# Performance work log

Measured on AMD Instinct MI355X. Metric: run time of the kernel, lower is better.

Reference implementation:

```python
import jax, jax.numpy as jnp
import numpy as np

N = 100000
NEG_SLOPE = 0.2

def _leaky_relu(x, slope):
    return jnp.where(x >= 0, x, slope * x)

def _gat_layer(h_in, W, a_src, a_dst, b, src, dst, heads, out_ch):
    # h: [N, H, C]
    h = (h_in @ W).reshape(-1, heads, out_ch)
    alpha_src = (h * a_src).sum(-1)  # [N, H]
    alpha_dst = (h * a_dst).sum(-1)  # [N, H]
    e = _leaky_relu(alpha_src[src] + alpha_dst[dst], NEG_SLOPE)  # [E, H]
    # segment softmax over destination nodes
    m = jax.ops.segment_max(e, dst, num_segments=N)
    m = jnp.where(jnp.isfinite(m), m, 0.0)
    ex = jnp.exp(e - m[dst])
    denom = jax.ops.segment_sum(ex, dst, num_segments=N)
    attn = ex / (denom[dst] + 1e-16)  # [E, H]
    out = jax.ops.segment_sum(h[src] * attn[:, :, None], dst, num_segments=N)  # [N, H, C]
    return out.reshape(-1, heads * out_ch) + b

def setup_inputs() -> dict:
    key = jax.random.key(0)
    ks = jax.random.split(key, 10)
    F_in, H1, C1, n_cls = 512, 8, 8, 16
    E = 1600000
    x = jax.random.normal(ks[0], (N, F_in), dtype=jnp.float32)
    edge_index = jax.random.randint(ks[1], (2, E), 0, N, dtype=jnp.int64)
    s1 = 1.0 / np.sqrt(F_in)
    W1 = jax.random.uniform(ks[2], (F_in, H1 * C1), jnp.float32, -s1, s1)
    a1_src = jax.random.normal(ks[3], (H1, C1), dtype=jnp.float32) * 0.1
    a1_dst = jax.random.normal(ks[4], (H1, C1), dtype=jnp.float32) * 0.1
    b1 = jnp.zeros((H1 * C1,), jnp.float32)
    s2 = 1.0 / np.sqrt(H1 * C1)
    W2 = jax.random.uniform(ks[5], (H1 * C1, n_cls), jnp.float32, -s2, s2)
    a2_src = jax.random.normal(ks[6], (1, n_cls), dtype=jnp.float32) * 0.1
    a2_dst = jax.random.normal(ks[7], (1, n_cls), dtype=jnp.float32) * 0.1
    b2 = jnp.zeros((n_cls,), jnp.float32)
    return {"x": x, "edge_index": edge_index, "W1": W1, "a1_src": a1_src,
            "a1_dst": a1_dst, "b1": b1, "W2": W2, "a2_src": a2_src,
            "a2_dst": a2_dst, "b2": b2}

def reference(x, edge_index, W1, a1_src, a1_dst, b1, W2, a2_src, a2_dst, b2):
    # add self loops (GATConv default)
    loops = jnp.arange(N, dtype=edge_index.dtype)
    src = jnp.concatenate([edge_index[0], loops])
    dst = jnp.concatenate([edge_index[1], loops])
    h = _gat_layer(x, W1, a1_src, a1_dst, b1, src, dst, 8, 8)
    h = jax.nn.elu(h)
    out = _gat_layer(h, W2, a2_src, a2_dst, b2, src, dst, 1, 16)
    return jax.nn.log_softmax(out, axis=1)
```

## Files before the change

### kernel.cpp

```cpp
#include <hip/hip_runtime.h>
#include <math.h>

#define NEG_SLOPE 0.2f
#define BKT_SHIFT 8
#define BKT_RANGE 256
#define EPB 4096

typedef __attribute__((ext_vector_type(8))) short bf16x8;
typedef __attribute__((ext_vector_type(4))) float f32x4;

__device__ __forceinline__ float elu1(float x)  { return x > 0.f ? x : expm1f(x); }

__device__ __forceinline__ unsigned short f2bf(float f) {
  unsigned u = __float_as_uint(f);
  unsigned r = (u + 0x7FFFu + ((u >> 16) & 1u)) >> 16;
  return (unsigned short)r;
}
__device__ __forceinline__ float bflo(unsigned u) { return __uint_as_float(u << 16); }
__device__ __forceinline__ float bfhi(unsigned u) { return __uint_as_float(u & 0xFFFF0000u); }
__device__ __forceinline__ unsigned cvt_pk_bf16(float lo, float hi) {
  unsigned r;
  asm("v_cvt_pk_bf16_f32 %0, %1, %2" : "=v"(r) : "v"(lo), "v"(hi));
  return r;
}

__global__ __launch_bounds__(256) void k_cvtW_zero(const float* __restrict__ W,
                                                   unsigned short* __restrict__ Wt,
                                                   int* __restrict__ bucketCount) {
  int i = blockIdx.x * 256 + threadIdx.x;
  if (i < 1024) bucketCount[i] = 0;
  if (i >= 512 * 64) return;
  int k = i >> 6, c = i & 63;
  Wt[(size_t)c * 512 + k] = f2bf(W[i]);
}

__global__ __launch_bounds__(256) void k_gemm1_mfma(const float* __restrict__ x,
                                                    const unsigned short* __restrict__ Wt,
                                                    const float* __restrict__ a1s,
                                                    const float* __restrict__ a1d,
                                                    unsigned* __restrict__ h1f8,
                                                    unsigned* __restrict__ ef1sp,
                                                    unsigned* __restrict__ ef1dp, int N) {
  __shared__ __align__(16) unsigned short As[128 * 64];
  __shared__ __align__(16) unsigned short Bs[64 * 64];
  const int t = threadIdx.x;
  const int w = t >> 6;
  const int l = t & 63;
  const int fr = l & 15;
  const int fq = l >> 4;
  const int rowbase = blockIdx.x * 128;
  f32x4 acc[2][4] = {};

  for (int k0 = 0; k0 < 512; k0 += 64) {
#pragma unroll
    for (int j = 0; j < 8; ++j) {
      int idx = j * 256 + t;
      int row = idx >> 4;
      int cg  = idx & 15;
      int grow = rowbase + row;
      float4 v = make_float4(0.f, 0.f, 0.f, 0.f);
      if (grow < N) v = *(const float4*)(x + (size_t)grow * 512 + k0 + cg * 4);
      uint2 pk;
      pk.x = cvt_pk_bf16(v.x, v.y);
      pk.y = cvt_pk_bf16(v.z, v.w);
      int ch = cg >> 1;
      int pch = ch ^ (row & 7);
      *((uint2*)(As + row * 64 + pch * 8 + (cg & 1) * 4)) = pk;
    }
#pragma unroll
    for (int rep = 0; rep < 2; ++rep) {
      int i = t + rep * 256;
      int c = i >> 3, ch = i & 7;
      uint4 v = *(const uint4*)(Wt + (size_t)c * 512 + k0 + ch * 8);
      *((uint4*)(Bs + c * 64 + (ch ^ (c & 7)) * 8)) = v;
    }
    __syncthreads();
#pragma unroll
    for (int ks = 0; ks < 2; ++ks) {
      bf16x8 a[2], b[4];
#pragma unroll
      for (int m = 0; m < 2; ++m) {
        int r = w * 32 + m * 16 + fr;
        int ch = (ks * 4 + fq) ^ (r & 7);
        a[m] = *((const bf16x8*)(As + r * 64 + ch * 8));
      }
#pragma unroll
      for (int n = 0; n < 4; ++n) {
        int c = n * 16 + fr;
        int ch = (ks * 4 + fq) ^ (c & 7);
        b[n] = *((const bf16x8*)(Bs + c * 64 + ch * 8));
      }
#pragma unroll
      for (int m = 0; m < 2; ++m)
#pragma unroll
        for (int n = 0; n < 4; ++n)
          acc[m][n] = __builtin_amdgcn_mfma_f32_16x16x32_bf16(a[m], b[n], acc[m][n], 0, 0, 0);
    }
    __syncthreads();
  }

  float* Asf = (float*)As;
#pragma unroll
  for (int m = 0; m < 2; ++m) {
    if (m) __syncthreads();
#pragma unroll
    for (int reg = 0; reg < 4; ++reg) {
      int lrow = w * 16 + fq * 4 + reg;
#pragma unroll
      for (int n = 0; n < 4; ++n)
        Asf[lrow * 64 + n * 16 + fr] = acc[m][n][reg];
    }
    __syncthreads();
#pragma unroll
    for (int p = 0; p < 4; ++p) {
      int flat = p * 256 + t;
      int lrow = flat >> 4, j = flat & 15;
      int g = rowbase + ((lrow >> 4) << 5) + m * 16 + (lrow & 15);
      float4 f = *(float4*)(Asf + lrow * 64 + j * 4);
      unsigned u = __builtin_amdgcn_cvt_pk_fp8_f32(f.x, f.y, 0u, 0);
      u = __builtin_amdgcn_cvt_pk_fp8_f32(f.z, f.w, u, 1);
      if (g < N) h1f8[(size_t)g * 16 + j] = u;
    }
#pragma unroll
    for (int p = 0; p < 2; ++p) {
      int flat = p * 256 + t;
      int lrow = flat >> 3, hh = flat & 7;
      int g = rowbase + ((lrow >> 4) << 5) + m * 16 + (lrow & 15);
      float4 f0 = *(float4*)(Asf + lrow * 64 + hh * 8);
      float4 f1 = *(float4*)(Asf + lrow * 64 + hh * 8 + 4);
      const float* sa = a1s + hh * 8;
      const float* da = a1d + hh * 8;
      float ss = f0.x*sa[0]+f0.y*sa[1]+f0.z*sa[2]+f0.w*sa[3]
               + f1.x*sa[4]+f1.y*sa[5]+f1.z*sa[6]+f1.w*sa[7];
      float dd = f0.x*da[0]+f0.y*da[1]+f0.z*da[2]+f0.w*da[3]
               + f1.x*da[4]+f1.y*da[5]+f1.z*da[6]+f1.w*da[7];
      if (g < N) {
        ef1sp[(size_t)g * 8 + hh] = cvt_pk_bf16(expf(ss), expf(NEG_SLOPE * ss));
        ef1dp[(size_t)g * 8 + hh] = cvt_pk_bf16(expf(dd), expf(NEG_SLOPE * dd));
      }
    }
  }
}

__global__ __launch_bounds__(256) void k_bhist(const int* __restrict__ dst,
                                               int* __restrict__ bucketCount,
                                               int E, int B) {
  __shared__ int h[512];
  int t = threadIdx.x;
  for (int i = t; i < B; i += 256) h[i] = 0;
  __syncthreads();
  int e0 = blockIdx.x * EPB;
#pragma unroll
  for (int i = 0; i < EPB / 256; ++i) {
    int e = e0 + i * 256 + t;
    if (e < E) atomicAdd(&h[dst[e] >> BKT_SHIFT], 1);
  }
  __syncthreads();
  for (int i = t; i < B; i += 256)
    if (h[i]) atomicAdd(bucketCount + i, h[i]);
}

__global__ __launch_bounds__(512) void k_bscan(const int* __restrict__ bucketCount,
                                               int* __restrict__ bucketOff,
                                               int* __restrict__ gCursor, int B, int E) {
  __shared__ int sm[512];
  int t = threadIdx.x;
  int v = (t < B) ? bucketCount[t] : 0;
  sm[t] = v;
  __syncthreads();
  int acc = v;
#pragma unroll
  for (int o = 1; o < 512; o <<= 1) {
    int u = (t >= o) ? sm[t - o] : 0;
    __syncthreads();
    acc += u;
    sm[t] = acc;
    __syncthreads();
  }
  if (t < B) {
    bucketOff[t] = acc - v;
    gCursor[t] = acc - v;
  }
  if (t == 0) bucketOff[B] = E;
}

__global__ __launch_bounds__(256) void k_bin(const int* __restrict__ src,
                                             const int* __restrict__ dst,
                                             int* __restrict__ gCursor,
                                             unsigned* __restrict__ binned,
                                             int E, int B) {
  __shared__ int hist[512];
  __shared__ int base[512];
  int t = threadIdx.x;
  for (int i = t; i < B; i += 256) hist[i] = 0;
  __syncthreads();
  int e0 = blockIdx.x * EPB;
#pragma unroll
  for (int i = 0; i < EPB / 256; ++i) {
    int e = e0 + i * 256 + t;
    if (e < E) atomicAdd(&hist[dst[e] >> BKT_SHIFT], 1);
  }
  __syncthreads();
  for (int i = t; i < B; i += 256) {
    int c = hist[i];
    base[i] = c ? atomicAdd(gCursor + i, c) : 0;
    hist[i] = 0;
  }
  __syncthreads();
#pragma unroll
  for (int i = 0; i < EPB / 256; ++i) {
    int e = e0 + i * 256 + t;
    if (e < E) {
      int d = dst[e];
      int b = d >> BKT_SHIFT;
      int r = atomicAdd(&hist[b], 1);
      binned[base[b] + r] = ((unsigned)(d & (BKT_RANGE - 1)) << 24) | (unsigned)src[e];
    }
  }
}

__global__ __launch_bounds__(256) void k_build(const int* __restrict__ bucketOff,
                                               const unsigned* __restrict__ binned,
                                               int* __restrict__ rowptr,
                                               int* __restrict__ deg,
                                               int* __restrict__ srt, int N) {
  __shared__ int ldeg[BKT_RANGE];
  __shared__ int sm[BKT_RANGE];
  __shared__ int lcur[BKT_RANGE];
  int t = threadIdx.x;
  int b = blockIdx.x;
  int nbase = b * BKT_RANGE;
  int estart = bucketOff[b];
  int eend = bucketOff[b + 1];
  ldeg[t] = 0;
  __syncthreads();
  for (int e = estart + t; e < eend; e += 256)
    atomicAdd(&ldeg[binned[e] >> 24], 1);
  __syncthreads();
  int v = ldeg[t];
  sm[t] = v;
  __syncthreads();
  int acc = v;
#pragma unroll
  for (int o = 1; o < 256; o <<= 1) {
    int u = (t >= o) ? sm[t - o] : 0;
    __syncthreads();
    acc += u;
    sm[t] = acc;
    __syncthreads();
  }
  int excl = estart + acc - v;
  int node = nbase + t;
  if (node < N) {
    rowptr[node] = excl;
    deg[node] = v;
  }
  lcur[t] = excl;
  __syncthreads();
  for (int e = estart + t; e < eend; e += 256) {
    unsigned p = binned[e];
    int pos = atomicAdd(&lcur[p >> 24], 1);
    srt[pos] = (int)(p & 0xFFFFFFu);
  }
}

__global__ __launch_bounds__(256) void k_agg1f(const int* __restrict__ rowptr,
                                               const int* __restrict__ deg,
                                               const int* __restrict__ srt,
                                               const unsigned* __restrict__ ef1sp,
                                               const unsigned* __restrict__ ef1dp,
                                               const unsigned* __restrict__ h1f8,
                                               const float* __restrict__ b1,
                                               const float* __restrict__ W2,
                                               const float* __restrict__ a2s,
                                               const float* __restrict__ a2d,
                                               unsigned short* __restrict__ h2b,
                                               unsigned* __restrict__ ef2sp,
                                               float* __restrict__ ef2d, int N) {
  __shared__ float vsm[4][64];
  const int t = threadIdx.x;
  const int w = t >> 6;
  const int lane = t & 63;
  const int wid = blockIdx.x * 4 + w;
  const int slot = lane >> 4;
  const int c4 = lane & 15;
  const int h = c4 >> 1;
  float a2sr = a2s[c4];
  float a2dr = a2d[c4];
  float wreg[16];
#pragma unroll
  for (int m = 0; m < 16; ++m) wreg[m] = W2[(slot * 16 + m) * 16 + c4];
  float4 b1v = *(const float4*)(b1 + c4 * 4);
  if (wid >= N) return;
  const int d = wid;

  unsigned ddu = ef1dp[(size_t)d * 8 + h];
  float ddx = bflo(ddu), ddy = bfhi(ddu);
  unsigned es0 = ef1sp[(size_t)d * 8 + h];
  unsigned sv = h1f8[(size_t)d * 16 + c4];
  float ex0 = fmaxf(bflo(es0) * ddx, bfhi(es0) * ddy);
  ex0 = (slot == 0) ? ex0 : 0.f;
  float a0 = ex0 * __builtin_amdgcn_cvt_f32_fp8(sv, 0);
  float a1 = ex0 * __builtin_amdgcn_cvt_f32_fp8(sv, 1);
  float a2 = ex0 * __builtin_amdgcn_cvt_f32_fp8(sv, 2);
  float a3 = ex0 * __builtin_amdgcn_cvt_f32_fp8(sv, 3);
  float den = ex0;

  int start = rowptr[d];
  int len = deg[d];
  for (int kb = 0; kb < len; kb += 64) {
    int li = kb + lane;
    int sreg = (li < len) ? srt[start + li] : 0;
    int nit = min(16, (len - kb + 3) >> 2);
#pragma unroll 2
    for (int it = 0; it < nit; ++it) {
      int idx = kb + it * 4 + slot;
      int s = __shfl(sreg, it * 4 + slot);
      bool valid = idx < len;
      unsigned es = ef1sp[(size_t)s * 8 + h];
      unsigned hv = h1f8[(size_t)s * 16 + c4];
      float ex = fmaxf(bflo(es) * ddx, bfhi(es) * ddy);
      ex = valid ? ex : 0.f;
      a0 = fmaf(ex, __builtin_amdgcn_cvt_f32_fp8(hv, 0), a0);
      a1 = fmaf(ex, __builtin_amdgcn_cvt_f32_fp8(hv, 1), a1);
      a2 = fmaf(ex, __builtin_amdgcn_cvt_f32_fp8(hv, 2), a2);
      a3 = fmaf(ex, __builtin_amdgcn_cvt_f32_fp8(hv, 3), a3);
      den += ex;
    }
  }
#pragma unroll
  for (int o = 16; o < 64; o <<= 1) {
    a0 += __shfl_xor(a0, o);
    a1 += __shfl_xor(a1, o);
    a2 += __shfl_xor(a2, o);
    a3 += __shfl_xor(a3, o);
    den += __shfl_xor(den, o);
  }
  float rden = 1.f / (den + 1e-16f);
  if (slot == 0) {
    float4 vv;
    vv.x = elu1(a0 * rden + b1v.x);
    vv.y = elu1(a1 * rden + b1v.y);
    vv.z = elu1(a2 * rden + b1v.z);
    vv.w = elu1(a3 * rden + b1v.w);
    *(float4*)&vsm[w][c4 * 4] = vv;
  }
  float partial = 0.f;
#pragma unroll
  for (int m = 0; m < 16; ++m) partial = fmaf(vsm[w][slot * 16 + m], wreg[m], partial);
  float qs = partial * a2sr;
  float qd = partial * a2dr;
#pragma unroll
  for (int o = 1; o < 64; o <<= 1) {
    qs += __shfl_xor(qs, o);
    qd += __shfl_xor(qd, o);
  }
  float p2 = partial + __shfl_down(partial, 32);
  float hcv = p2 + __shfl_down(p2, 16);
  if (lane < 16) h2b[(size_t)d * 16 + c4] = f2bf(hcv);
  if (lane == 0) {
    ef2sp[d] = cvt_pk_bf16(expf(qs), expf(NEG_SLOPE * qs));
    *(float2*)(ef2d + (size_t)d * 2) = make_float2(expf(qd), expf(NEG_SLOPE * qd));
  }
}

__global__ __launch_bounds__(256) void k_agg2(const int* __restrict__ rowptr,
                                              const int* __restrict__ deg,
                                              const int* __restrict__ srt,
                                              const unsigned* __restrict__ ef2sp,
                                              const float* __restrict__ ef2d,
                                              const unsigned short* __restrict__ h2b,
                                              const float* __restrict__ b2,
                                              float* __restrict__ out, int N) {
  const int t = threadIdx.x;
  const int lane = t & 63;
  const int wid = (blockIdx.x * 256 + t) >> 6;
  const int slot = lane >> 2;
  const int cg = lane & 3;
  float4 b2v = *(const float4*)(b2 + cg * 4);
  if (wid >= N) return;
  const int d = wid;
  float2 ddp = *(const float2*)(ef2d + (size_t)d * 2);
  unsigned ps0 = ef2sp[d];
  uint2 sv = *(const uint2*)(h2b + (size_t)d * 16 + cg * 4);
  float ex0 = fmaxf(bflo(ps0) * ddp.x, bfhi(ps0) * ddp.y);
  ex0 = (slot == 0) ? ex0 : 0.f;
  float a0 = ex0 * bflo(sv.x), a1 = ex0 * bfhi(sv.x);
  float a2 = ex0 * bflo(sv.y), a3 = ex0 * bfhi(sv.y);
  float den = ex0;

  int start = rowptr[d];
  int len = deg[d];
  for (int kb = 0; kb < len; kb += 64) {
    int li = kb + lane;
    int sreg = (li < len) ? srt[start + li] : 0;
    int nit = min(4, (len - kb + 15) >> 4);
#pragma unroll 2
    for (int it = 0; it < nit; ++it) {
      int idx = kb + it * 16 + slot;
      int s = __shfl(sreg, it * 16 + slot);
      bool valid = idx < len;
      unsigned ps = ef2sp[s];
      uint2 hv = *(const uint2*)(h2b + (size_t)s * 16 + cg * 4);
      float ex = fmaxf(bflo(ps) * ddp.x, bfhi(ps) * ddp.y);
      ex = valid ? ex : 0.f;
      a0 = fmaf(ex, bflo(hv.x), a0);
      a1 = fmaf(ex, bfhi(hv.x), a1);
      a2 = fmaf(ex, bflo(hv.y), a2);
      a3 = fmaf(ex, bfhi(hv.y), a3);
      den += ex;
    }
  }
#pragma unroll
  for (int o = 4; o < 64; o <<= 1) {
    a0 += __shfl_xor(a0, o);
    a1 += __shfl_xor(a1, o);
    a2 += __shfl_xor(a2, o);
    a3 += __shfl_xor(a3, o);
    den += __shfl_xor(den, o);
  }
  float rden = 1.f / (den + 1e-16f);
  float v0 = a0 * rden + b2v.x;
  float v1 = a1 * rden + b2v.y;
  float v2 = a2 * rden + b2v.z;
  float v3 = a3 * rden + b2v.w;
  float m = fmaxf(fmaxf(v0, v1), fmaxf(v2, v3));
  m = fmaxf(m, __shfl_xor(m, 1));
  m = fmaxf(m, __shfl_xor(m, 2));
  float s = expf(v0 - m) + expf(v1 - m) + expf(v2 - m) + expf(v3 - m);
  s += __shfl_xor(s, 1);
  s += __shfl_xor(s, 2);
  float lse = m + logf(s);
  if (lane < 4) {
    float4 o4 = make_float4(v0 - lse, v1 - lse, v2 - lse, v3 - lse);
    *(float4*)(out + (size_t)d * 16 + cg * 4) = o4;
  }
}

extern "C" void kernel_launch(void* const* d_in, const int* in_sizes, int n_in,
                              void* d_out, int out_size, void* d_ws, size_t ws_size,
                              hipStream_t stream) {
  const float* x    = (const float*)d_in[0];
  const int*   ei   = (const int*)d_in[1];
  const float* W1   = (const float*)d_in[2];
  const float* a1s  = (const float*)d_in[3];
  const float* a1d  = (const float*)d_in[4];
  const float* b1   = (const float*)d_in[5];
  const float* W2   = (const float*)d_in[6];
  const float* a2s  = (const float*)d_in[7];
  const float* a2d  = (const float*)d_in[8];
  const float* b2   = (const float*)d_in[9];
  float* out = (float*)d_out;

  const int N = in_sizes[0] / 512;
  const int E = in_sizes[1] / 2;
  const int* src = ei;
  const int* dst = ei + E;
  const int B = (N + BKT_RANGE - 1) >> BKT_SHIFT;
  const int EB = (E + EPB - 1) / EPB;

  float* w = (float*)d_ws;
  float* ef2d = w;  w += (size_t)N * 2;
  unsigned* ef1sp = (unsigned*)w;  w += (size_t)N * 8;
  unsigned* ef1dp = (unsigned*)w;  w += (size_t)N * 8;
  unsigned* ef2sp = (unsigned*)w;  w += (size_t)N;
  unsigned* h1f8  = (unsigned*)w;  w += (size_t)N * 16;
  unsigned short* h2b = (unsigned short*)w;  w += (size_t)N * 8;
  unsigned short* Wt  = (unsigned short*)w;  w += 512 * 64 / 2;
  int* iw = (int*)w;
  int* deg         = iw;  iw += N;
  int* rowptr      = iw;  iw += N;
  int* bucketCount = iw;  iw += 1024;
  int* bucketOff   = iw;  iw += 1024;
  int* gCursor     = iw;  iw += 1024;
  int* srt         = iw;  iw += E;
  unsigned* binned = (unsigned*)iw;  iw += E;

  k_cvtW_zero<<<(512 * 64 + 255) / 256, 256, 0, stream>>>(W1, Wt, bucketCount);

  k_bhist<<<EB, 256, 0, stream>>>(dst, bucketCount, E, B);
  k_bscan<<<1, 512, 0, stream>>>(bucketCount, bucketOff, gCursor, B, E);
  k_bin<<<EB, 256, 0, stream>>>(src, dst, gCursor, binned, E, B);
  k_build<<<B, 256, 0, stream>>>(bucketOff, binned, rowptr, deg, srt, N);

  k_gemm1_mfma<<<(N + 127) / 128, 256, 0, stream>>>(x, Wt, a1s, a1d, h1f8, ef1sp, ef1dp, N);
  k_agg1f<<<(N + 3) / 4, 256, 0, stream>>>(rowptr, deg, srt, ef1sp, ef1dp, h1f8,
                                           b1, W2, a2s, a2d, h2b, ef2sp, ef2d, N);

  k_agg2<<<(N + 3) / 4, 256, 0, stream>>>(rowptr, deg, srt, ef2sp, ef2d, h2b, b2, out, N);
}
```

Baseline: 222.6 us.

## Interleave source attention and features, load GEMM A directly, fold bucket scan

Four separate changes. The GEMM now loads x rows straight into MFMA A-fragment registers instead of staging them through shared memory, which shrinks the LDS footprint. The per-source attention exponentials and the fp8 features are packed into one 24-word record per node, so each gathered edge in aggregation touches a single 96-byte region instead of two separate arrays. The standalone bucket scan kernel is removed and every k_bin and k_build block recomputes the prefix sum in shared memory, trading redundant work for one fewer launch; aggregation loops also get a higher unroll factor.

Result: faster. 212.0 us (-4.8%).

```diff
diff --git a/kernel.cpp b/kernel.cpp
--- a/kernel.cpp
+++ b/kernel.cpp
@@ -38,11 +38,11 @@
                                                     const unsigned short* __restrict__ Wt,
                                                     const float* __restrict__ a1s,
                                                     const float* __restrict__ a1d,
-                                                    unsigned* __restrict__ h1f8,
-                                                    unsigned* __restrict__ ef1sp,
+                                                    unsigned* __restrict__ hx,
                                                     unsigned* __restrict__ ef1dp, int N) {
-  __shared__ __align__(16) unsigned short As[128 * 64];
-  __shared__ __align__(16) unsigned short Bs[64 * 64];
+  __shared__ __align__(16) float Sm[64 * 64];
+  unsigned short* Bs = (unsigned short*)Sm;
+  float* Asf = Sm;
   const int t = threadIdx.x;
   const int w = t >> 6;
   const int l = t & 63;
@@ -51,22 +51,13 @@
   const int rowbase = blockIdx.x * 128;
   f32x4 acc[2][4] = {};
 
+  const int r0g = rowbase + w * 32 + fr;
+  const int r1g = r0g + 16;
+  const bool v0 = r0g < N, v1 = r1g < N;
+  const float* xr0 = x + (size_t)r0g * 512 + fq * 8;
+  const float* xr1 = x + (size_t)r1g * 512 + fq * 8;
+
   for (int k0 = 0; k0 < 512; k0 += 64) {
-#pragma unroll
-    for (int j = 0; j < 8; ++j) {
-      int idx = j * 256 + t;
-      int row = idx >> 4;
-      int cg  = idx & 15;
-      int grow = rowbase + row;
-      float4 v = make_float4(0.f, 0.f, 0.f, 0.f);
-      if (grow < N) v = *(const float4*)(x + (size_t)grow * 512 + k0 + cg * 4);
-      uint2 pk;
-      pk.x = cvt_pk_bf16(v.x, v.y);
-      pk.y = cvt_pk_bf16(v.z, v.w);
-      int ch = cg >> 1;
-      int pch = ch ^ (row & 7);
-      *((uint2*)(As + row * 64 + pch * 8 + (cg & 1) * 4)) = pk;
-    }
 #pragma unroll
     for (int rep = 0; rep < 2; ++rep) {
       int i = t + rep * 256;
@@ -74,16 +65,30 @@
       uint4 v = *(const uint4*)(Wt + (size_t)c * 512 + k0 + ch * 8);
       *((uint4*)(Bs + c * 64 + (ch ^ (c & 7)) * 8)) = v;
     }
+    bf16x8 a[2][2];
+#pragma unroll
+    for (int m = 0; m < 2; ++m) {
+      const float* xr = m ? xr1 : xr0;
+      bool vv = m ? v1 : v0;
+#pragma unroll
+      for (int ks = 0; ks < 2; ++ks) {
+        float4 f0 = make_float4(0.f, 0.f, 0.f, 0.f), f1 = f0;
+        if (vv) {
+          f0 = *(const float4*)(xr + k0 + ks * 32);
+          f1 = *(const float4*)(xr + k0 + ks * 32 + 4);
+        }
+        union { unsigned u[4]; bf16x8 v8; } un;
+        un.u[0] = cvt_pk_bf16(f0.x, f0.y);
+        un.u[1] = cvt_pk_bf16(f0.z, f0.w);
+        un.u[2] = cvt_pk_bf16(f1.x, f1.y);
+        un.u[3] = cvt_pk_bf16(f1.z, f1.w);
+        a[m][ks] = un.v8;
+      }
+    }
     __syncthreads();
 #pragma unroll
     for (int ks = 0; ks < 2; ++ks) {
-      bf16x8 a[2], b[4];
-#pragma unroll
-      for (int m = 0; m < 2; ++m) {
-        int r = w * 32 + m * 16 + fr;
-        int ch = (ks * 4 + fq) ^ (r & 7);
-        a[m] = *((const bf16x8*)(As + r * 64 + ch * 8));
-      }
+      bf16x8 b[4];
 #pragma unroll
       for (int n = 0; n < 4; ++n) {
         int c = n * 16 + fr;
@@ -94,12 +99,11 @@
       for (int m = 0; m < 2; ++m)
 #pragma unroll
         for (int n = 0; n < 4; ++n)
-          acc[m][n] = __builtin_amdgcn_mfma_f32_16x16x32_bf16(a[m], b[n], acc[m][n], 0, 0, 0);
-    }
-    __syncthreads();
-  }
-
-  float* Asf = (float*)As;
+          acc[m][n] = __builtin_amdgcn_mfma_f32_16x16x32_bf16(a[m][ks], b[n], acc[m][n], 0, 0, 0);
+    }
+    __syncthreads();
+  }
+
 #pragma unroll
   for (int m = 0; m < 2; ++m) {
     if (m) __syncthreads();
@@ -119,7 +123,7 @@
       float4 f = *(float4*)(Asf + lrow * 64 + j * 4);
       unsigned u = __builtin_amdgcn_cvt_pk_fp8_f32(f.x, f.y, 0u, 0);
       u = __builtin_amdgcn_cvt_pk_fp8_f32(f.z, f.w, u, 1);
-      if (g < N) h1f8[(size_t)g * 16 + j] = u;
+      if (g < N) hx[(size_t)g * 24 + 8 + j] = u;
     }
 #pragma unroll
     for (int p = 0; p < 2; ++p) {
@@ -135,7 +139,7 @@
       float dd = f0.x*da[0]+f0.y*da[1]+f0.z*da[2]+f0.w*da[3]
                + f1.x*da[4]+f1.y*da[5]+f1.z*da[6]+f1.w*da[7];
       if (g < N) {
-        ef1sp[(size_t)g * 8 + hh] = cvt_pk_bf16(expf(ss), expf(NEG_SLOPE * ss));
+        hx[(size_t)g * 24 + hh] = cvt_pk_bf16(expf(ss), expf(NEG_SLOPE * ss));
         ef1dp[(size_t)g * 8 + hh] = cvt_pk_bf16(expf(dd), expf(NEG_SLOPE * dd));
       }
     }
@@ -160,40 +164,28 @@
     if (h[i]) atomicAdd(bucketCount + i, h[i]);
 }
 
-__global__ __launch_bounds__(512) void k_bscan(const int* __restrict__ bucketCount,
-                                               int* __restrict__ bucketOff,
-                                               int* __restrict__ gCursor, int B, int E) {
-  __shared__ int sm[512];
-  int t = threadIdx.x;
-  int v = (t < B) ? bucketCount[t] : 0;
-  sm[t] = v;
-  __syncthreads();
-  int acc = v;
-#pragma unroll
-  for (int o = 1; o < 512; o <<= 1) {
-    int u = (t >= o) ? sm[t - o] : 0;
-    __syncthreads();
-    acc += u;
-    sm[t] = acc;
-    __syncthreads();
-  }
-  if (t < B) {
-    bucketOff[t] = acc - v;
-    gCursor[t] = acc - v;
-  }
-  if (t == 0) bucketOff[B] = E;
-}
-
 __global__ __launch_bounds__(256) void k_bin(const int* __restrict__ src,
                                              const int* __restrict__ dst,
-                                             int* __restrict__ gCursor,
+                                             const int* __restrict__ bucketCount,
+                                             int* __restrict__ gCursorRel,
                                              unsigned* __restrict__ binned,
                                              int E, int B) {
+  __shared__ int sc[512];
   __shared__ int hist[512];
   __shared__ int base[512];
   int t = threadIdx.x;
-  for (int i = t; i < B; i += 256) hist[i] = 0;
-  __syncthreads();
+  sc[t]       = (t < B) ? bucketCount[t] : 0;
+  sc[t + 256] = (t + 256 < B) ? bucketCount[t + 256] : 0;
+  for (int i = t; i < 512; i += 256) hist[i] = 0;
+  __syncthreads();
+  for (int o = 1; o < 512; o <<= 1) {
+    int a0 = (t >= o) ? sc[t - o] : 0;
+    int a1 = (t + 256 >= o) ? sc[t + 256 - o] : 0;
+    __syncthreads();
+    sc[t] += a0;
+    sc[t + 256] += a1;
+    __syncthreads();
+  }
   int e0 = blockIdx.x * EPB;
 #pragma unroll
   for (int i = 0; i < EPB / 256; ++i) {
@@ -203,7 +195,8 @@
   __syncthreads();
   for (int i = t; i < B; i += 256) {
     int c = hist[i];
-    base[i] = c ? atomicAdd(gCursor + i, c) : 0;
+    int excl = sc[i] - bucketCount[i];
+    base[i] = c ? (excl + atomicAdd(gCursorRel + i, c)) : 0;
     hist[i] = 0;
   }
   __syncthreads();
@@ -219,21 +212,32 @@
   }
 }
 
-__global__ __launch_bounds__(256) void k_build(const int* __restrict__ bucketOff,
+__global__ __launch_bounds__(256) void k_build(const int* __restrict__ bucketCount,
                                                const unsigned* __restrict__ binned,
                                                int* __restrict__ rowptr,
                                                int* __restrict__ deg,
-                                               int* __restrict__ srt, int N) {
+                                               int* __restrict__ srt, int N, int B) {
+  __shared__ int sc[512];
   __shared__ int ldeg[BKT_RANGE];
   __shared__ int sm[BKT_RANGE];
   __shared__ int lcur[BKT_RANGE];
   int t = threadIdx.x;
   int b = blockIdx.x;
+  sc[t]       = (t < B) ? bucketCount[t] : 0;
+  sc[t + 256] = (t + 256 < B) ? bucketCount[t + 256] : 0;
+  ldeg[t] = 0;
+  __syncthreads();
+  for (int o = 1; o < 512; o <<= 1) {
+    int a0 = (t >= o) ? sc[t - o] : 0;
+    int a1 = (t + 256 >= o) ? sc[t + 256 - o] : 0;
+    __syncthreads();
+    sc[t] += a0;
+    sc[t + 256] += a1;
+    __syncthreads();
+  }
+  int eend = sc[b];
+  int estart = eend - bucketCount[b];
   int nbase = b * BKT_RANGE;
-  int estart = bucketOff[b];
-  int eend = bucketOff[b + 1];
-  ldeg[t] = 0;
-  __syncthreads();
   for (int e = estart + t; e < eend; e += 256)
     atomicAdd(&ldeg[binned[e] >> 24], 1);
   __syncthreads();
@@ -267,9 +271,8 @@
 __global__ __launch_bounds__(256) void k_agg1f(const int* __restrict__ rowptr,
                                                const int* __restrict__ deg,
                                                const int* __restrict__ srt,
-                                               const unsigned* __restrict__ ef1sp,
+                                               const unsigned* __restrict__ hx,
                                                const unsigned* __restrict__ ef1dp,
-                                               const unsigned* __restrict__ h1f8,
                                                const float* __restrict__ b1,
                                                const float* __restrict__ W2,
                                                const float* __restrict__ a2s,
@@ -296,8 +299,8 @@
 
   unsigned ddu = ef1dp[(size_t)d * 8 + h];
   float ddx = bflo(ddu), ddy = bfhi(ddu);
-  unsigned es0 = ef1sp[(size_t)d * 8 + h];
-  unsigned sv = h1f8[(size_t)d * 16 + c4];
+  unsigned es0 = hx[(size_t)d * 24 + h];
+  unsigned sv = hx[(size_t)d * 24 + 8 + c4];
   float ex0 = fmaxf(bflo(es0) * ddx, bfhi(es0) * ddy);
   ex0 = (slot == 0) ? ex0 : 0.f;
   float a0 = ex0 * __builtin_amdgcn_cvt_f32_fp8(sv, 0);
@@ -312,13 +315,13 @@
     int li = kb + lane;
     int sreg = (li < len) ? srt[start + li] : 0;
     int nit = min(16, (len - kb + 3) >> 2);
-#pragma unroll 2
+#pragma unroll 4
     for (int it = 0; it < nit; ++it) {
       int idx = kb + it * 4 + slot;
       int s = __shfl(sreg, it * 4 + slot);
       bool valid = idx < len;
-      unsigned es = ef1sp[(size_t)s * 8 + h];
-      unsigned hv = h1f8[(size_t)s * 16 + c4];
+      unsigned es = hx[(size_t)s * 24 + h];
+      unsigned hv = hx[(size_t)s * 24 + 8 + c4];
       float ex = fmaxf(bflo(es) * ddx, bfhi(es) * ddy);
       ex = valid ? ex : 0.f;
       a0 = fmaf(ex, __builtin_amdgcn_cvt_f32_fp8(hv, 0), a0);
@@ -395,7 +398,7 @@
     int li = kb + lane;
     int sreg = (li < len) ? srt[start + li] : 0;
     int nit = min(4, (len - kb + 15) >> 4);
-#pragma unroll 2
+#pragma unroll 4
     for (int it = 0; it < nit; ++it) {
       int idx = kb + it * 16 + slot;
       int s = __shfl(sreg, it * 16 + slot);
@@ -461,30 +464,27 @@
 
   float* w = (float*)d_ws;
   float* ef2d = w;  w += (size_t)N * 2;
-  unsigned* ef1sp = (unsigned*)w;  w += (size_t)N * 8;
   unsigned* ef1dp = (unsigned*)w;  w += (size_t)N * 8;
   unsigned* ef2sp = (unsigned*)w;  w += (size_t)N;
-  unsigned* h1f8  = (unsigned*)w;  w += (size_t)N * 16;
+  unsigned* hx    = (unsigned*)w;  w += (size_t)N * 24;
   unsigned short* h2b = (unsigned short*)w;  w += (size_t)N * 8;
   unsigned short* Wt  = (unsigned short*)w;  w += 512 * 64 / 2;
   int* iw = (int*)w;
   int* deg         = iw;  iw += N;
   int* rowptr      = iw;  iw += N;
-  int* bucketCount = iw;  iw += 1024;
-  int* bucketOff   = iw;  iw += 1024;
-  int* gCursor     = iw;  iw += 1024;
+  int* bucketCount = iw;  iw += 512;
+  int* gCursorRel  = iw;  iw += 512;
   int* srt         = iw;  iw += E;
   unsigned* binned = (unsigned*)iw;  iw += E;
 
   k_cvtW_zero<<<(512 * 64 + 255) / 256, 256, 0, stream>>>(W1, Wt, bucketCount);
 
   k_bhist<<<EB, 256, 0, stream>>>(dst, bucketCount, E, B);
-  k_bscan<<<1, 512, 0, stream>>>(bucketCount, bucketOff, gCursor, B, E);
-  k_bin<<<EB, 256, 0, stream>>>(src, dst, gCursor, binned, E, B);
-  k_build<<<B, 256, 0, stream>>>(bucketOff, binned, rowptr, deg, srt, N);
-
-  k_gemm1_mfma<<<(N + 127) / 128, 256, 0, stream>>>(x, Wt, a1s, a1d, h1f8, ef1sp, ef1dp, N);
-  k_agg1f<<<(N + 3) / 4, 256, 0, stream>>>(rowptr, deg, srt, ef1sp, ef1dp, h1f8,
+  k_bin<<<EB, 256, 0, stream>>>(src, dst, bucketCount, gCursorRel, binned, E, B);
+  k_build<<<B, 256, 0, stream>>>(bucketCount, binned, rowptr, deg, srt, N, B);
+
+  k_gemm1_mfma<<<(N + 127) / 128, 256, 0, stream>>>(x, Wt, a1s, a1d, hx, ef1dp, N);
+  k_agg1f<<<(N + 3) / 4, 256, 0, stream>>>(rowptr, deg, srt, hx, ef1dp,
                                            b1, W2, a2s, a2d, h2b, ef2sp, ef2d, N);
 
   k_agg2<<<(N + 3) / 4, 256, 0, stream>>>(rowptr, deg, srt, ef2sp, ef2d, h2b, b2, out, N);
```
